# Kernel optimization log

Measured on AMD Instinct MI355X. Metric: run time of the kernel, lower is better.

The kernel has to match this reference:

```python
import jax, jax.numpy as jnp
import numpy as np

B, V, E, L, D = 4, 64, 1024, 1024, 256  # batch, vertices, edges/graph, seq_len, d_model
DEG = E // V


def setup_inputs() -> dict:
    key = jax.random.key(0)
    k0, k1, k2, k3, k4, k5 = jax.random.split(key, 6)
    # fixed 16-regular graph, edges sorted by (src, dst) so that nonzero()
    # extraction order of the dense adjacency equals a gather at (src, dst)
    src = np.repeat(np.arange(V), DEG)
    dst = (src + 1 + np.tile(np.arange(DEG), V)) % V
    order = np.lexsort((dst, src))
    src, dst = src[order], dst[order]
    edge_index = jnp.asarray(np.stack([np.tile(src, B), np.tile(dst, B)]), dtype=jnp.int32)
    hidden_states = jax.random.normal(k0, (B * V, L, D), dtype=jnp.float32)
    edge_weight = jax.random.uniform(k1, (B * E,), dtype=jnp.float32, minval=0.1, maxval=1.0)
    s = 0.02
    Wq = jax.random.normal(k2, (D, D), dtype=jnp.float32) * s
    bq = jax.random.normal(k3, (D,), dtype=jnp.float32) * s
    Wk = jax.random.normal(k4, (D, D), dtype=jnp.float32) * s
    bk = jax.random.normal(k5, (D,), dtype=jnp.float32) * s
    attn_skip = jnp.float32(0.5)
    return {"hidden_states": hidden_states, "edge_index": edge_index, "edge_weight": edge_weight,
            "Wq": Wq, "bq": bq, "Wk": Wk, "bk": bk, "attn_skip": attn_skip}


def reference(hidden_states, edge_index, edge_weight, Wq, bq, Wk, bk, attn_skip):
    # broadcast static edge list / weights across time, as the torch repeat does
    ei = jnp.broadcast_to(edge_index[:, :, None], (2, B * E, L))
    ew = jnp.broadcast_to(edge_weight[:, None], (B * E, L))
    hs = hidden_states.reshape(B, V, L, D)
    Q = hs @ Wq.T + bq  # nn.Linear: x W^T + b
    K = hs @ Wk.T + bk
    att = jnp.einsum('bvld,bwld->bvwl', Q, K) / jnp.sqrt(jnp.float32(D))
    bidx = jnp.repeat(jnp.arange(B), E)
    src, dst = edge_index[0], edge_index[1]
    # to_dense_adj: scatter-add edge weights -> (B, V, V, L)
    adj = jnp.zeros((B, V, V, L), att.dtype).at[bidx, src, dst, :].add(ew)
    mask = jnp.where(adj > 0, 0.0, -jnp.inf)
    att = jax.nn.softmax(att + mask, axis=2)  # softmax over destination vertices w
    adj_new = attn_skip * adj + (1.0 - attn_skip) * att
    # dense_to_sparse: nonzeros in (graph=b*L+l, row, col) row-major order.
    # Edges are sorted by (src,dst), so this is a gather; torch flat order is (b, l, e):
    g = adj_new[bidx, src, dst, :]  # (B*E, L) ordered (b, e, l)
    flat = g.reshape(B, E, L).transpose(0, 2, 1).reshape(-1)  # order (b, l, e)
    # replicate the original .view(B, E, L).transpose(1, 2).reshape(B*E, L)
    ew_out = flat.reshape(B, E, L).transpose(0, 2, 1).reshape(B * E, L)
    return ei, ew_out
```

## Files before the change

### kernel.cpp

```cpp
#include <hip/hip_runtime.h>
#include <cstdint>
#include <cstddef>

constexpr int Bv = 4;
constexpr int Ev = 1024;
constexpr int Lv = 1024;
constexpr int BE = Bv * Ev;
constexpr size_t EI_PLANE = (size_t)BE * Lv;

constexpr int STRB = 264;

typedef __bf16 bf16x8 __attribute__((ext_vector_type(8)));
typedef __bf16 bf16x4 __attribute__((ext_vector_type(4)));
typedef __bf16 bf16x2 __attribute__((ext_vector_type(2)));
typedef float  f32x4  __attribute__((ext_vector_type(4)));

static __device__ __forceinline__ unsigned int pack_bf2(float lo, float hi) {
    union { bf16x2 h; unsigned int u; } c;
    c.h[0] = (__bf16)lo; c.h[1] = (__bf16)hi;
    return c.u;
}

__global__ __launch_bounds__(256) void precompute_kernel(
    const float* __restrict__ Wq, const float* __restrict__ Wk,
    const float* __restrict__ bq, __bf16* __restrict__ Mb, float* __restrict__ rv)
{
    const int blk = blockIdx.x;
    const int tid = threadIdx.x;
    if (blk < 256) {
        __shared__ float qs[256 * 17];
        __shared__ float ks[256 * 17];
        const int i16 = (blk >> 4) * 16;
        const int j16 = (blk & 15) * 16;
        const int c  = tid & 15;
        const int r0 = tid >> 4;
        #pragma unroll
        for (int it = 0; it < 16; ++it) {
            const int r = it * 16 + r0;
            qs[r * 17 + c] = Wq[r * 256 + i16 + c];
            ks[r * 17 + c] = Wk[r * 256 + j16 + c];
        }
        __syncthreads();
        const int dd = tid >> 4;
        const int tt = tid & 15;
        float a0 = 0.f, a1 = 0.f, a2 = 0.f, a3 = 0.f;
        for (int r = 0; r < 256; r += 4) {
            a0 = fmaf(qs[(r + 0) * 17 + dd], ks[(r + 0) * 17 + tt], a0);
            a1 = fmaf(qs[(r + 1) * 17 + dd], ks[(r + 1) * 17 + tt], a1);
            a2 = fmaf(qs[(r + 2) * 17 + dd], ks[(r + 2) * 17 + tt], a2);
            a3 = fmaf(qs[(r + 3) * 17 + dd], ks[(r + 3) * 17 + tt], a3);
        }
        const float m = ((a0 + a1) + (a2 + a3)) * 0.0625f;
        const int d = i16 + dd, t = j16 + tt;
        const int f    = (d >> 5) * 16 + (t >> 4);
        const int lane = ((d >> 3) & 3) * 16 + (t & 15);
        const int jj   = d & 7;
        Mb[((size_t)f * 64 + lane) * 8 + jj] = (__bf16)m;
    } else {
        __shared__ float bqs[256];
        bqs[tid] = bq[tid];
        __syncthreads();
        float a0 = 0.f, a1 = 0.f;
        for (int i = 0; i < 256; i += 2) {
            a0 = fmaf(bqs[i + 0], Wk[(i + 0) * 256 + tid], a0);
            a1 = fmaf(bqs[i + 1], Wk[(i + 1) * 256 + tid], a1);
        }
        rv[tid] = (a0 + a1) * 0.0625f;
    }
}

template <bool USE_WS>
__global__ __launch_bounds__(256) void edge_main(
    const float* __restrict__ hs, const int* __restrict__ eidx,
    const float* __restrict__ ew, const float* __restrict__ skipp,
    const __bf16* __restrict__ Mb, const float* __restrict__ rv,
    float* __restrict__ probs_or_out)
{
    __shared__ __bf16 hs_s[64 * STRB];
    float* S0 = (float*)hs_s;
    float* S1 = S0 + 2304;

    const int bl = blockIdx.x;
    const int b  = bl >> 10;
    const int l  = bl & 1023;
    const int tid  = threadIdx.x;
    const int w    = tid >> 6;
    const int lane = tid & 63;
    const int l15  = lane & 15;
    const int quad = lane >> 4;

    {
        const float* base = hs + ((size_t)b * 64 * 1024 + (size_t)l) * 256;
        const int half = lane >> 5;
        const int c8   = (lane & 31) * 8;
        #pragma unroll
        for (int k = 0; k < 8; ++k) {
            const int v = k * 8 + w * 2 + half;
            const float* p = base + (size_t)v * (1024 * 256) + c8;
            float4 va = *(const float4*)p;
            float4 vb = *(const float4*)(p + 4);
            bf16x8 h;
            h[0] = (__bf16)va.x; h[1] = (__bf16)va.y;
            h[2] = (__bf16)va.z; h[3] = (__bf16)va.w;
            h[4] = (__bf16)vb.x; h[5] = (__bf16)vb.y;
            h[6] = (__bf16)vb.z; h[7] = (__bf16)vb.w;
            *(bf16x8*)(&hs_s[v * STRB + c8]) = h;
        }
    }
    __syncthreads();

    f32x4 s_acc[4][2];
    #pragma unroll
    for (int mt = 0; mt < 4; ++mt)
        #pragma unroll
        for (int sl = 0; sl < 2; ++sl) {
            s_acc[mt][sl][0] = 0.f; s_acc[mt][sl][1] = 0.f;
            s_acc[mt][sl][2] = 0.f; s_acc[mt][sl][3] = 0.f;
        }

    #pragma unroll 1
    for (int cch = 0; cch < 2; ++cch) {
        #pragma unroll
        for (int mtg = 0; mtg < 2; ++mtg) {
            f32x4 acc[2][2];
            #pragma unroll
            for (int tt = 0; tt < 2; ++tt) {
                const f32x4 rb = *(const f32x4*)(rv + cch * 128 + w * 32 + tt * 16 + quad * 4);
                acc[tt][0] = rb;
                acc[tt][1] = rb;
            }
            #pragma unroll
            for (int kt = 0; kt < 8; ++kt) {
                bf16x8 mfr[2];
                #pragma unroll
                for (int tt = 0; tt < 2; ++tt)
                    mfr[tt] = *(const bf16x8*)(Mb +
                        ((size_t)(kt * 16 + cch * 8 + w * 2 + tt) * 64 + lane) * 8);
                #pragma unroll
                for (int mi = 0; mi < 2; ++mi) {
                    const bf16x8 hfr = *(const bf16x8*)(
                        &hs_s[((mtg * 2 + mi) * 16 + l15) * STRB + kt * 32 + quad * 8]);
                    acc[0][mi] = __builtin_amdgcn_mfma_f32_16x16x32_bf16(
                        mfr[0], hfr, acc[0][mi], 0, 0, 0);
                    acc[1][mi] = __builtin_amdgcn_mfma_f32_16x16x32_bf16(
                        mfr[1], hfr, acc[1][mi], 0, 0, 0);
                }
            }
            #pragma unroll
            for (int mi = 0; mi < 2; ++mi) {
                const int mt = mtg * 2 + mi;
                unsigned int Ar = pack_bf2(acc[0][mi][0], acc[0][mi][1]);
                unsigned int Br = pack_bf2(acc[0][mi][2], acc[0][mi][3]);
                unsigned int Cr = pack_bf2(acc[1][mi][0], acc[1][mi][1]);
                unsigned int Dr = pack_bf2(acc[1][mi][2], acc[1][mi][3]);
                asm("v_permlane32_swap_b32 %0, %1" : "+v"(Ar), "+v"(Cr));
                asm("v_permlane16_swap_b32 %0, %1" : "+v"(Ar), "+v"(Cr));
                asm("v_permlane32_swap_b32 %0, %1" : "+v"(Br), "+v"(Dr));
                asm("v_permlane16_swap_b32 %0, %1" : "+v"(Br), "+v"(Dr));
                union { uint4 u; bf16x8 h; } fr;
                fr.u = make_uint4(Ar, Br, Cr, Dr);
                const bf16x8 browa = *(const bf16x8*)(
                    &hs_s[(mt * 16 + l15) * STRB + cch * 128 + w * 32 + quad * 8]);
                const bf16x8 browb = *(const bf16x8*)(
                    &hs_s[(((mt + 1) & 3) * 16 + l15) * STRB + cch * 128 + w * 32 + quad * 8]);
                s_acc[mt][0] = __builtin_amdgcn_mfma_f32_16x16x32_bf16(
                    fr.h, browa, s_acc[mt][0], 0, 0, 0);
                s_acc[mt][1] = __builtin_amdgcn_mfma_f32_16x16x32_bf16(
                    fr.h, browb, s_acc[mt][1], 0, 0, 0);
            }
        }
    }
    __syncthreads();

    {
        float* Sbuf = (w & 2) ? S1 : S0;
        if (!(w & 1)) {
            #pragma unroll
            for (int mt = 0; mt < 4; ++mt)
                #pragma unroll
                for (int sl = 0; sl < 2; ++sl)
                    #pragma unroll
                    for (int r = 0; r < 4; ++r)
                        Sbuf[(mt * 16 + quad * 4 + r) * 36 + sl * 16 + l15] =
                            s_acc[mt][sl][r];
        }
        __syncthreads();
        if (w & 1) {
            #pragma unroll
            for (int mt = 0; mt < 4; ++mt)
                #pragma unroll
                for (int sl = 0; sl < 2; ++sl)
                    #pragma unroll
                    for (int r = 0; r < 4; ++r)
                        Sbuf[(mt * 16 + quad * 4 + r) * 36 + sl * 16 + l15] +=
                            s_acc[mt][sl][r];
        }
        __syncthreads();
        #pragma unroll
        for (int k2 = 0; k2 < 9; ++k2)
            S0[k2 * 256 + tid] += S1[k2 * 256 + tid];
        __syncthreads();
    }

    const int e0  = tid * 4;
    const int be0 = b * Ev + e0;
    int srcs[4], dsts[4];
    #pragma unroll
    for (int j = 0; j < 4; ++j) {
        srcs[j] = eidx[be0 + j];
        dsts[j] = eidx[BE + be0 + j];
    }
    float lg[4];
    #pragma unroll
    for (int j = 0; j < 4; ++j) {
        const int slot = ((dsts[j] >> 4) - (srcs[j] >> 4)) & 3;
        lg[j] = S0[srcs[j] * 36 + slot * 16 + (dsts[j] & 15)];
    }

    float mx = fmaxf(fmaxf(lg[0], lg[1]), fmaxf(lg[2], lg[3]));
    mx = fmaxf(mx, __shfl_xor(mx, 1));
    mx = fmaxf(mx, __shfl_xor(mx, 2));
    float ex[4], sm = 0.f;
    #pragma unroll
    for (int j = 0; j < 4; ++j) { ex[j] = __expf(lg[j] - mx); sm += ex[j]; }
    sm += __shfl_xor(sm, 1);
    sm += __shfl_xor(sm, 2);
    const float inv = 1.0f / sm;

    if (USE_WS) {
        float4 o = make_float4(ex[0] * inv, ex[1] * inv, ex[2] * inv, ex[3] * inv);
        *(float4*)(probs_or_out + (size_t)bl * 1024 + e0) = o;
    } else {
        const float skip = skipp[0];
        const float om = 1.0f - skip;
        #pragma unroll
        for (int j = 0; j < 4; ++j) {
            float g = fmaf(skip, ew[be0 + j], om * (ex[j] * inv));
            probs_or_out[(size_t)(be0 + j) * Lv + l] = g;
        }
    }
}

__global__ __launch_bounds__(256) void output_kernel(
    const float* __restrict__ probs, const int* __restrict__ eidx,
    const float* __restrict__ ew, const float* __restrict__ skipp,
    float* __restrict__ out)
{
    __shared__ float tile[64 * 68];
    const int lt = blockIdx.x;
    const int et = blockIdx.y;
    const int b  = blockIdx.z;
    const int t  = threadIdx.x;
    const int tr = t >> 4;
    const int tc = t & 15;

    #pragma unroll
    for (int q = 0; q < 4; ++q) {
        const int lloc = q * 16 + tr;
        float4 v = *(const float4*)(probs +
            ((size_t)(b * 1024 + lt * 64 + lloc)) * 1024 + et * 64 + tc * 4);
        *(float4*)(&tile[lloc * 68 + tc * 4]) = v;
    }
    __syncthreads();

    const float skip = skipp[0];
    const float om = 1.0f - skip;
    float* out_ei0 = out;
    float* out_ei1 = out + EI_PLANE;
    float* out_ew  = out + 2 * EI_PLANE;

    #pragma unroll
    for (int q = 0; q < 4; ++q) {
        const int eloc = q * 16 + tr;
        const int be = b * Ev + et * 64 + eloc;
        const float w  = ew[be];
        const float sv = (float)eidx[be];
        const float dv = (float)eidx[BE + be];
        const int lloc0 = tc * 4;
        float4 o;
        o.x = fmaf(skip, w, om * tile[(lloc0 + 0) * 68 + eloc]);
        o.y = fmaf(skip, w, om * tile[(lloc0 + 1) * 68 + eloc]);
        o.z = fmaf(skip, w, om * tile[(lloc0 + 2) * 68 + eloc]);
        o.w = fmaf(skip, w, om * tile[(lloc0 + 3) * 68 + eloc]);
        const size_t off = (size_t)be * Lv + lt * 64 + lloc0;
        *(float4*)(out_ew  + off) = o;
        *(float4*)(out_ei0 + off) = make_float4(sv, sv, sv, sv);
        *(float4*)(out_ei1 + off) = make_float4(dv, dv, dv, dv);
    }
}

__global__ __launch_bounds__(256) void ei_kernel(
    const int* __restrict__ eidx, float* __restrict__ out)
{
    const int blk = blockIdx.x;
    const int c = blk >> 12;
    const int j = blk & 4095;
    const float v = (float)eidx[c * BE + j];
    float4 o = make_float4(v, v, v, v);
    *(float4*)(out + (size_t)blk * 1024 + threadIdx.x * 4) = o;
}

extern "C" void kernel_launch(void* const* d_in, const int* in_sizes, int n_in,
                              void* d_out, int out_size, void* d_ws, size_t ws_size,
                              hipStream_t stream)
{
    const float* hs   = (const float*)d_in[0];
    const int*   eidx = (const int*)d_in[1];
    const float* ew   = (const float*)d_in[2];
    const float* Wq   = (const float*)d_in[3];
    const float* bq   = (const float*)d_in[4];
    const float* Wk   = (const float*)d_in[5];
    const float* skip = (const float*)d_in[7];

    char* wsb = (char*)d_ws;
    __bf16* Mb   = (__bf16*)wsb;
    float*  rv   = (float*)(wsb + 131072);
    float*  probs = (float*)(wsb + 132096);
    const size_t need = 132096 + (size_t)Bv * Lv * Ev * sizeof(float);

    precompute_kernel<<<dim3(257), dim3(256), 0, stream>>>(Wq, Wk, bq, Mb, rv);

    if (ws_size >= need) {
        edge_main<true><<<dim3(Bv * Lv), dim3(256), 0, stream>>>(
            hs, eidx, ew, skip, Mb, rv, probs);
        output_kernel<<<dim3(16, 16, 4), dim3(256), 0, stream>>>(
            probs, eidx, ew, skip, (float*)d_out);
    } else {
        float* out_ew = (float*)d_out + 2 * EI_PLANE;
        edge_main<false><<<dim3(Bv * Lv), dim3(256), 0, stream>>>(
            hs, eidx, ew, skip, Mb, rv, out_ew);
        ei_kernel<<<dim3(2 * BE), dim3(256), 0, stream>>>(eidx, (float*)d_out);
    }
}
```

Before: 433.9 us.

## Repartition MFMA work across waves by vertex tiles to shrink score reduction

Each wave now owns two vertex row tiles and half of the projected feature chunks, instead of all four vertex tiles for a quarter of the features. This halves the per-wave score accumulators and replaces the four-way cross-wave reduction (two LDS buffers plus an extra sum pass and barrier) with a two-way store/add into a single buffer. The cost is that each wave loads the M fragments for twice as many feature chunks, though it runs fewer MFMAs per chunk, so total MFMA count is unchanged while global/L2 traffic for the weights rises.

```diff
diff --git a/kernel.cpp b/kernel.cpp
--- a/kernel.cpp
+++ b/kernel.cpp
@@ -78,7 +78,6 @@
 {
     __shared__ __bf16 hs_s[64 * STRB];
     float* S0 = (float*)hs_s;
-    float* S1 = S0 + 2304;
 
     const int bl = blockIdx.x;
     const int b  = bl >> 10;
@@ -88,6 +87,8 @@
     const int lane = tid & 63;
     const int l15  = lane & 15;
     const int quad = lane >> 4;
+    const int vgrp  = w >> 1;
+    const int thalf = w & 1;
 
     {
         const float* base = hs + ((size_t)b * 64 * 1024 + (size_t)l) * 256;
@@ -109,98 +110,90 @@
     }
     __syncthreads();
 
-    f32x4 s_acc[4][2];
-    #pragma unroll
-    for (int mt = 0; mt < 4; ++mt)
+    f32x4 s_acc[2][2];
+    #pragma unroll
+    for (int mi = 0; mi < 2; ++mi)
         #pragma unroll
         for (int sl = 0; sl < 2; ++sl) {
-            s_acc[mt][sl][0] = 0.f; s_acc[mt][sl][1] = 0.f;
-            s_acc[mt][sl][2] = 0.f; s_acc[mt][sl][3] = 0.f;
-        }
+            s_acc[mi][sl][0] = 0.f; s_acc[mi][sl][1] = 0.f;
+            s_acc[mi][sl][2] = 0.f; s_acc[mi][sl][3] = 0.f;
+        }
+
+    const int vt0 = vgrp * 2;
 
     #pragma unroll 1
-    for (int cch = 0; cch < 2; ++cch) {
-        #pragma unroll
-        for (int mtg = 0; mtg < 2; ++mtg) {
-            f32x4 acc[2][2];
-            #pragma unroll
-            for (int tt = 0; tt < 2; ++tt) {
-                const f32x4 rb = *(const f32x4*)(rv + cch * 128 + w * 32 + tt * 16 + quad * 4);
-                acc[tt][0] = rb;
-                acc[tt][1] = rb;
-            }
-            #pragma unroll
-            for (int kt = 0; kt < 8; ++kt) {
-                bf16x8 mfr[2];
-                #pragma unroll
-                for (int tt = 0; tt < 2; ++tt)
-                    mfr[tt] = *(const bf16x8*)(Mb +
-                        ((size_t)(kt * 16 + cch * 8 + w * 2 + tt) * 64 + lane) * 8);
-                #pragma unroll
-                for (int mi = 0; mi < 2; ++mi) {
-                    const bf16x8 hfr = *(const bf16x8*)(
-                        &hs_s[((mtg * 2 + mi) * 16 + l15) * STRB + kt * 32 + quad * 8]);
-                    acc[0][mi] = __builtin_amdgcn_mfma_f32_16x16x32_bf16(
-                        mfr[0], hfr, acc[0][mi], 0, 0, 0);
-                    acc[1][mi] = __builtin_amdgcn_mfma_f32_16x16x32_bf16(
-                        mfr[1], hfr, acc[1][mi], 0, 0, 0);
-                }
-            }
+    for (int pp = 0; pp < 4; ++pp) {
+        const int p = thalf * 4 + pp;
+        f32x4 acc[2][2];
+        #pragma unroll
+        for (int tt = 0; tt < 2; ++tt) {
+            const f32x4 rb = *(const f32x4*)(rv + (2 * p + tt) * 16 + quad * 4);
+            acc[tt][0] = rb;
+            acc[tt][1] = rb;
+        }
+        #pragma unroll
+        for (int kt = 0; kt < 8; ++kt) {
+            const bf16x8 mfr0 = *(const bf16x8*)(Mb +
+                ((size_t)((kt * 16 + 2 * p + 0) * 64 + lane)) * 8);
+            const bf16x8 mfr1 = *(const bf16x8*)(Mb +
+                ((size_t)((kt * 16 + 2 * p + 1) * 64 + lane)) * 8);
             #pragma unroll
             for (int mi = 0; mi < 2; ++mi) {
-                const int mt = mtg * 2 + mi;
-                unsigned int Ar = pack_bf2(acc[0][mi][0], acc[0][mi][1]);
-                unsigned int Br = pack_bf2(acc[0][mi][2], acc[0][mi][3]);
-                unsigned int Cr = pack_bf2(acc[1][mi][0], acc[1][mi][1]);
-                unsigned int Dr = pack_bf2(acc[1][mi][2], acc[1][mi][3]);
-                asm("v_permlane32_swap_b32 %0, %1" : "+v"(Ar), "+v"(Cr));
-                asm("v_permlane16_swap_b32 %0, %1" : "+v"(Ar), "+v"(Cr));
-                asm("v_permlane32_swap_b32 %0, %1" : "+v"(Br), "+v"(Dr));
-                asm("v_permlane16_swap_b32 %0, %1" : "+v"(Br), "+v"(Dr));
-                union { uint4 u; bf16x8 h; } fr;
-                fr.u = make_uint4(Ar, Br, Cr, Dr);
-                const bf16x8 browa = *(const bf16x8*)(
-                    &hs_s[(mt * 16 + l15) * STRB + cch * 128 + w * 32 + quad * 8]);
-                const bf16x8 browb = *(const bf16x8*)(
-                    &hs_s[(((mt + 1) & 3) * 16 + l15) * STRB + cch * 128 + w * 32 + quad * 8]);
-                s_acc[mt][0] = __builtin_amdgcn_mfma_f32_16x16x32_bf16(
-                    fr.h, browa, s_acc[mt][0], 0, 0, 0);
-                s_acc[mt][1] = __builtin_amdgcn_mfma_f32_16x16x32_bf16(
-                    fr.h, browb, s_acc[mt][1], 0, 0, 0);
+                const bf16x8 hfr = *(const bf16x8*)(
+                    &hs_s[((vt0 + mi) * 16 + l15) * STRB + kt * 32 + quad * 8]);
+                acc[0][mi] = __builtin_amdgcn_mfma_f32_16x16x32_bf16(
+                    mfr0, hfr, acc[0][mi], 0, 0, 0);
+                acc[1][mi] = __builtin_amdgcn_mfma_f32_16x16x32_bf16(
+                    mfr1, hfr, acc[1][mi], 0, 0, 0);
             }
         }
-    }
-    __syncthreads();
-
-    {
-        float* Sbuf = (w & 2) ? S1 : S0;
-        if (!(w & 1)) {
+        #pragma unroll
+        for (int mi = 0; mi < 2; ++mi) {
+            const int m = vt0 + mi;
+            unsigned int Ar = pack_bf2(acc[0][mi][0], acc[0][mi][1]);
+            unsigned int Br = pack_bf2(acc[0][mi][2], acc[0][mi][3]);
+            unsigned int Cr = pack_bf2(acc[1][mi][0], acc[1][mi][1]);
+            unsigned int Dr = pack_bf2(acc[1][mi][2], acc[1][mi][3]);
+            asm("v_permlane32_swap_b32 %0, %1" : "+v"(Ar), "+v"(Cr));
+            asm("v_permlane16_swap_b32 %0, %1" : "+v"(Ar), "+v"(Cr));
+            asm("v_permlane32_swap_b32 %0, %1" : "+v"(Br), "+v"(Dr));
+            asm("v_permlane16_swap_b32 %0, %1" : "+v"(Br), "+v"(Dr));
+            union { uint4 u; bf16x8 h; } fr;
+            fr.u = make_uint4(Ar, Br, Cr, Dr);
+            const bf16x8 brow0 = *(const bf16x8*)(
+                &hs_s[(m * 16 + l15) * STRB + p * 32 + quad * 8]);
+            const bf16x8 brow1 = *(const bf16x8*)(
+                &hs_s[(((m + 1) & 3) * 16 + l15) * STRB + p * 32 + quad * 8]);
+            s_acc[mi][0] = __builtin_amdgcn_mfma_f32_16x16x32_bf16(
+                fr.h, brow0, s_acc[mi][0], 0, 0, 0);
+            s_acc[mi][1] = __builtin_amdgcn_mfma_f32_16x16x32_bf16(
+                fr.h, brow1, s_acc[mi][1], 0, 0, 0);
+        }
+    }
+    __syncthreads();
+
+    if (!thalf) {
+        #pragma unroll
+        for (int mi = 0; mi < 2; ++mi)
             #pragma unroll
-            for (int mt = 0; mt < 4; ++mt)
+            for (int sl = 0; sl < 2; ++sl)
                 #pragma unroll
-                for (int sl = 0; sl < 2; ++sl)
-                    #pragma unroll
-                    for (int r = 0; r < 4; ++r)
-                        Sbuf[(mt * 16 + quad * 4 + r) * 36 + sl * 16 + l15] =
-                            s_acc[mt][sl][r];
-        }
-        __syncthreads();
-        if (w & 1) {
+                for (int r = 0; r < 4; ++r)
+                    S0[((vt0 + mi) * 16 + quad * 4 + r) * 36 + sl * 16 + l15] =
+                        s_acc[mi][sl][r];
+    }
+    __syncthreads();
+    if (thalf) {
+        #pragma unroll
+        for (int mi = 0; mi < 2; ++mi)
             #pragma unroll
-            for (int mt = 0; mt < 4; ++mt)
+            for (int sl = 0; sl < 2; ++sl)
                 #pragma unroll
-                for (int sl = 0; sl < 2; ++sl)
-                    #pragma unroll
-                    for (int r = 0; r < 4; ++r)
-                        Sbuf[(mt * 16 + quad * 4 + r) * 36 + sl * 16 + l15] +=
-                            s_acc[mt][sl][r];
-        }
-        __syncthreads();
-        #pragma unroll
-        for (int k2 = 0; k2 < 9; ++k2)
-            S0[k2 * 256 + tid] += S1[k2 * 256 + tid];
-        __syncthreads();
-    }
+                for (int r = 0; r < 4; ++r)
+                    S0[((vt0 + mi) * 16 + quad * 4 + r) * 36 + sl * 16 + l15] +=
+                        s_acc[mi][sl][r];
+    }
+    __syncthreads();
 
     const int e0  = tid * 4;
     const int be0 = b * Ev + e0;
```

Measured after the change: 445.0 us. 1.03x slower.
